# Performance work log

Measured on AMD Instinct MI355X. Metric: run time of the kernel, lower is better.

## Reference

```python
import jax, jax.numpy as jnp
import numpy as np

B, S, R, C_Q, C_KV, H, C_A = 1, 128, 256, 256, 256, 8, 32


def setup_inputs() -> dict:
    key = jax.random.key(0)
    ks = jax.random.split(key, 11)
    scale = 0.02
    q = jax.random.normal(ks[0], (B, S, R, C_Q), jnp.float32)
    kv = jax.random.normal(ks[1], (B, S, R, C_KV), jnp.float32)
    bias = jax.random.normal(ks[2], (B, 1, R, R, H), jnp.float32)
    bias_mask = jax.random.randint(ks[3], (B, S, R), 0, 2).astype(jnp.float32)
    w_q = jax.random.normal(ks[4], (C_Q, H, C_A), jnp.float32) * scale
    w_k = jax.random.normal(ks[5], (C_KV, H, C_A), jnp.float32) * scale
    w_v = jax.random.normal(ks[6], (C_KV, H, C_A), jnp.float32) * scale
    w_g = jax.random.normal(ks[7], (C_Q, H, C_A), jnp.float32) * scale
    b_g = jax.random.normal(ks[8], (H, C_A), jnp.float32) * scale
    w_o = jax.random.normal(ks[9], (H, C_A, C_Q), jnp.float32) * scale
    b_o = jax.random.normal(ks[10], (C_Q,), jnp.float32) * scale
    return {"q": q, "kv": kv, "bias": bias, "bias_mask": bias_mask,
            "w_q": w_q, "w_k": w_k, "w_v": w_v, "w_g": w_g, "b_g": b_g,
            "w_o": w_o, "b_o": b_o}


def reference(q, kv, bias, bias_mask, w_q, w_k, w_v, w_g, b_g, w_o, b_o):
    # q, kv: [B, S, R, C]; attention over residue dim R within each row s.
    c_a = w_q.shape[-1]
    normsize = 1.0 / jnp.sqrt(jnp.asarray(c_a, q.dtype))
    Q = jnp.einsum('bsqc,chd->bsqhd', q, w_q) * normsize  # [B,S,R,H,Ca]
    K = jnp.einsum('bskc,chd->bskhd', kv, w_k)
    V = jnp.einsum('bskc,chd->bskhd', kv, w_v)
    # affinity: [B,S,Q,K,H]
    AT = jnp.einsum('bsqhd,bskhd->bsqkh', Q, K)
    mask_bias = (bias_mask[:, :, None, :, None] - 1.0) * 1e9  # [B,S,1,K,1]
    AT = AT + bias + mask_bias
    AT = jax.nn.softmax(AT, axis=-2)  # softmax over K
    O = jnp.einsum('bsqkh,bskhd->bsqhd', AT, V)
    G = jax.nn.sigmoid(jnp.einsum('bsqc,chd->bsqhd', q, w_g) + b_g)
    O = O * G
    out = jnp.einsum('bsqhd,hdc->bsqc', O, w_o) + b_o  # [B,S,R,C_Q]
    return out
```

## Files before the change

### kernel.cpp

```cpp
#include <hip/hip_runtime.h>

typedef __bf16 bf16;
typedef __bf16 bf16x8 __attribute__((ext_vector_type(8)));
typedef __bf16 bf16x4 __attribute__((ext_vector_type(4)));
typedef float  f32x4  __attribute__((ext_vector_type(4)));
typedef unsigned int u32;
typedef unsigned int u32x2 __attribute__((ext_vector_type(2)));
typedef unsigned int u32x4 __attribute__((ext_vector_type(4)));
typedef unsigned short u16;

#define MFMA16(a, b, c) __builtin_amdgcn_mfma_f32_16x16x32_bf16((a), (b), (c), 0, 0, 0)
#define L2E 1.4426950408889634f


typedef __attribute__((address_space(3))) u32 lds_u32;
typedef const __attribute__((address_space(1))) u32 glob_u32;
__device__ __forceinline__ void gll16(const void* g, void* l) {
    __builtin_amdgcn_global_load_lds((glob_u32*)g, (lds_u32*)l, 16, 0, 0);
}

__device__ __forceinline__ u32 pk2(float lo, float hi) {
    u16 a = __builtin_bit_cast(u16, (bf16)lo);
    u16 b = __builtin_bit_cast(u16, (bf16)hi);
    return ((u32)b << 16) | (u32)a;
}

__device__ __forceinline__ bf16x8 cvt8(float4 a, float4 b) {
    bf16x8 t;
    t[0]=(bf16)a.x; t[1]=(bf16)a.y; t[2]=(bf16)a.z; t[3]=(bf16)a.w;
    t[4]=(bf16)b.x; t[5]=(bf16)b.y; t[6]=(bf16)b.z; t[7]=(bf16)b.w;
    return t;
}

__device__ __forceinline__ float fexp2(float x) {
#if __has_builtin(__builtin_amdgcn_exp2f)
    return __builtin_amdgcn_exp2f(x);
#else
    return exp2f(x);
#endif
}
__device__ __forceinline__ float frcp(float x) {
#if __has_builtin(__builtin_amdgcn_rcpf)
    return __builtin_amdgcn_rcpf(x);
#else
    return 1.0f / x;
#endif
}

__global__ __launch_bounds__(256) void prep_kernel(
    const float* __restrict__ bias,
    const float* __restrict__ w_q, const float* __restrict__ w_k,
    const float* __restrict__ w_v, const float* __restrict__ w_g,
    const float* __restrict__ w_o, const float* __restrict__ b_g,
    float* __restrict__ biasT,
    bf16* __restrict__ Wqg, bf16* __restrict__ Wkv, bf16* __restrict__ Wo,
    float* __restrict__ b_gL)
{
    const float norm = 0.17677669529663687f * L2E;
    const int gid = blockIdx.x * 256 + threadIdx.x;
    const int gsz = gridDim.x * 256;

    for (int u = gid; u < 524288; u += gsz) {
        int h = u >> 16, qq = (u >> 8) & 255, kk = u & 255;
        biasT[u] = bias[(((qq << 8) + kk) << 3) + h] * L2E;
    }
    for (int u = gid; u < 131072; u += gsz) {
        int n = u >> 8, k = u & 255;
        float v = (n < 256) ? w_q[k * 256 + n] * norm : w_g[k * 256 + (n - 256)] * L2E;
        Wqg[u] = (bf16)v;
    }
    for (int u = gid; u < 131072; u += gsz) {
        int n = u >> 8, k = u & 255;
        float v = (n < 256) ? w_k[k * 256 + n] : w_v[k * 256 + (n - 256)];
        Wkv[u] = (bf16)v;
    }
    for (int u = gid; u < 65536; u += gsz) {
        int n = u >> 8, k = u & 255;
        Wo[u] = (bf16)w_o[k * 256 + n];
    }
    for (int u = gid; u < 256; u += gsz) b_gL[u] = b_g[u] * L2E;
}

__device__ __forceinline__ void proj_core(
    const float* __restrict__ A32, const bf16* __restrict__ Bw,
    bf16* __restrict__ Cb, int m0, int n0)
{
    __shared__ __align__(16) bf16 As0[128 * 32], Bs0[128 * 32];
    __shared__ __align__(16) bf16 As1[128 * 32], Bs1[128 * 32];

    const int tid  = threadIdx.x;
    const int lane = tid & 63, wave = tid >> 6;
    const int quad = lane >> 4, lc = lane & 15;
    const int wr = wave >> 1, wc = wave & 1;

    const int r0 = tid >> 2, p0 = tid & 3;
    const size_t offA0 = (size_t)(m0 + r0) * 256 + p0 * 8;
    const size_t offA1 = (size_t)(m0 + 64 + r0) * 256 + p0 * 8;
    const bf16* gB0 = Bw + (size_t)(n0 + r0) * 256 + p0 * 8;
    const bf16* gB1 = Bw + (size_t)(n0 + 64 + r0) * 256 + p0 * 8;

    f32x4 acc[4][4];
    #pragma unroll
    for (int i = 0; i < 4; ++i)
        #pragma unroll
        for (int j = 0; j < 4; ++j) acc[i][j] = f32x4{0.f, 0.f, 0.f, 0.f};

    {
        float4 x0 = *(const float4*)(A32 + offA0);
        float4 x1 = *(const float4*)(A32 + offA0 + 4);
        float4 y0 = *(const float4*)(A32 + offA1);
        float4 y1 = *(const float4*)(A32 + offA1 + 4);
        *(bf16x8*)(As0 + tid * 8)         = cvt8(x0, x1);
        *(bf16x8*)(As0 + (tid + 256) * 8) = cvt8(y0, y1);
        gll16(gB0, Bs0 + tid * 8);
        gll16(gB1, Bs0 + (tid + 256) * 8);
    }
    __syncthreads();

    auto step = [&](const bf16* Ac, const bf16* Bc, bf16* An, bf16* Bn,
                    int kn, bool pf) {
        float4 x0, x1, y0, y1;
        if (pf) {
            x0 = *(const float4*)(A32 + offA0 + kn);
            x1 = *(const float4*)(A32 + offA0 + kn + 4);
            y0 = *(const float4*)(A32 + offA1 + kn);
            y1 = *(const float4*)(A32 + offA1 + kn + 4);
            gll16(gB0 + kn, Bn + tid * 8);
            gll16(gB1 + kn, Bn + (tid + 256) * 8);
        }
        __builtin_amdgcn_sched_barrier(0);

        bf16x8 aF[4], bF[4];
        #pragma unroll
        for (int mt = 0; mt < 4; ++mt)
            aF[mt] = *(const bf16x8*)(Ac + (wr * 64 + mt * 16 + lc) * 32 + quad * 8);
        #pragma unroll
        for (int nt = 0; nt < 4; ++nt)
            bF[nt] = *(const bf16x8*)(Bc + (wc * 64 + nt * 16 + lc) * 32 + quad * 8);
        #pragma unroll
        for (int mt = 0; mt < 4; ++mt)
            #pragma unroll
            for (int nt = 0; nt < 4; ++nt)
                acc[mt][nt] = MFMA16(aF[mt], bF[nt], acc[mt][nt]);

        if (pf) {
            *(bf16x8*)(An + tid * 8)         = cvt8(x0, x1);
            *(bf16x8*)(An + (tid + 256) * 8) = cvt8(y0, y1);
        }
        __syncthreads();
    };

    step(As0, Bs0, As1, Bs1,  32, true);
    step(As1, Bs1, As0, Bs0,  64, true);
    step(As0, Bs0, As1, Bs1,  96, true);
    step(As1, Bs1, As0, Bs0, 128, true);
    step(As0, Bs0, As1, Bs1, 160, true);
    step(As1, Bs1, As0, Bs0, 192, true);
    step(As0, Bs0, As1, Bs1, 224, true);
    step(As1, Bs1, As0, Bs0,   0, false);

    #pragma unroll
    for (int mt = 0; mt < 4; ++mt) {
        #pragma unroll
        for (int nt = 0; nt < 4; ++nt) {
            const int row = m0 + wr * 64 + mt * 16 + quad * 4;
            const int col = n0 + wc * 64 + nt * 16 + lc;
            #pragma unroll
            for (int rr = 0; rr < 4; ++rr)
                Cb[(size_t)(row + rr) * 512 + col] = (bf16)acc[mt][nt][rr];
        }
    }
}

__global__ __launch_bounds__(256) void proj_kernel(
    const float* __restrict__ qf, const float* __restrict__ kvf,
    const bf16* __restrict__ Wqg, const bf16* __restrict__ Wkv,
    bf16* __restrict__ QG, bf16* __restrict__ KV)
{
    int bid = blockIdx.x;
    bool sel = bid >= 1024;
    int b = bid & 1023;
    int strip = ((b >> 3) & 1) | ((b & 7) << 1) | (((b >> 4) & 15) << 4);
    int m0 = strip * 128, n0 = (b >> 8) * 128;
    proj_core(sel ? kvf : qf, sel ? Wkv : Wqg, sel ? KV : QG, m0, n0);
}

__global__ __launch_bounds__(256) void outproj_kernel(
    const bf16* __restrict__ OG, const bf16* __restrict__ Wo,
    const float* __restrict__ bo, float* __restrict__ out)
{
    __shared__ __align__(16) bf16 As0[64 * 32], Bs0[128 * 32];
    __shared__ __align__(16) bf16 As1[64 * 32], Bs1[128 * 32];

    const int bid = blockIdx.x;
    const int x = bid & 7;
    const int strip = ((bid >> 3) & 3) | (x << 2) | (((bid >> 5) & 15) << 5);
    const int m0 = strip * 64, n0 = (bid >> 9) * 128;

    const int tid  = threadIdx.x;
    const int lane = tid & 63, wave = tid >> 6;
    const int quad = lane >> 4, lc = lane & 15;
    const int wr = wave >> 1, wc = wave & 1;

    const int r0 = tid >> 2, p0 = tid & 3;
    const bf16* gA  = OG + (size_t)(m0 + r0) * 256 + p0 * 8;
    const bf16* gB0 = Wo + (size_t)(n0 + r0) * 256 + p0 * 8;
    const bf16* gB1 = Wo + (size_t)(n0 + 64 + r0) * 256 + p0 * 8;

    f32x4 acc[2][4];
    #pragma unroll
    for (int i = 0; i < 2; ++i)
        #pragma unroll
        for (int j = 0; j < 4; ++j) acc[i][j] = f32x4{0.f, 0.f, 0.f, 0.f};

    gll16(gA,  As0 + tid * 8);
    gll16(gB0, Bs0 + tid * 8);
    gll16(gB1, Bs0 + (tid + 256) * 8);
    __syncthreads();

    auto step = [&](const bf16* Ac, const bf16* Bc, bf16* An, bf16* Bn,
                    int kn, bool pf) {
        if (pf) {
            gll16(gA + kn,  An + tid * 8);
            gll16(gB0 + kn, Bn + tid * 8);
            gll16(gB1 + kn, Bn + (tid + 256) * 8);
        }
        __builtin_amdgcn_sched_barrier(0);

        bf16x8 aF[2], bF[4];
        #pragma unroll
        for (int mt = 0; mt < 2; ++mt)
            aF[mt] = *(const bf16x8*)(Ac + (wr * 32 + mt * 16 + lc) * 32 + quad * 8);
        #pragma unroll
        for (int nt = 0; nt < 4; ++nt)
            bF[nt] = *(const bf16x8*)(Bc + (wc * 64 + nt * 16 + lc) * 32 + quad * 8);
        #pragma unroll
        for (int mt = 0; mt < 2; ++mt)
            #pragma unroll
            for (int nt = 0; nt < 4; ++nt)
                acc[mt][nt] = MFMA16(aF[mt], bF[nt], acc[mt][nt]);
        __syncthreads();
    };

    step(As0, Bs0, As1, Bs1,  32, true);
    step(As1, Bs1, As0, Bs0,  64, true);
    step(As0, Bs0, As1, Bs1,  96, true);
    step(As1, Bs1, As0, Bs0, 128, true);
    step(As0, Bs0, As1, Bs1, 160, true);
    step(As1, Bs1, As0, Bs0, 192, true);
    step(As0, Bs0, As1, Bs1, 224, true);
    step(As1, Bs1, As0, Bs0,   0, false);

    #pragma unroll
    for (int mt = 0; mt < 2; ++mt) {
        #pragma unroll
        for (int nt = 0; nt < 4; ++nt) {
            const int row = m0 + wr * 32 + mt * 16 + quad * 4;
            const int col = n0 + wc * 64 + nt * 16 + lc;
            const float bb = bo[col];
            #pragma unroll
            for (int rr = 0; rr < 4; ++rr)
                out[(size_t)(row + rr) * 256 + col] = acc[mt][nt][rr] + bb;
        }
    }
}

#define A_OFF_MASK 0
#define A_OFF_K    1024
#define A_OFF_VT   21504
#define A_LDS_TOT  (21504 + 32 * 264 * 2)

__global__ __launch_bounds__(256) void attn_kernel(
    const bf16* __restrict__ QG, const bf16* __restrict__ KV,
    const float* __restrict__ biasT, const float* __restrict__ bias_mask,
    const float* __restrict__ b_gL, bf16* __restrict__ OG)
{
    __shared__ __align__(16) char smem[A_LDS_TOT];
    float* maskadd = (float*)(smem + A_OFF_MASK);
    bf16*  Ks      = (bf16*)(smem + A_OFF_K);
    bf16*  Vt      = (bf16*)(smem + A_OFF_VT);

    const int tid  = threadIdx.x;
    const int wave = tid >> 6, lane = tid & 63;
    const int quad = lane >> 4, lc = lane & 15;
    const int h = blockIdx.x >> 7;
    const int s = blockIdx.x & 127;

    maskadd[tid] = (bias_mask[s * 256 + tid] - 1.0f) * (1e9f * L2E);
    {
        const bf16* kvrow = KV + (size_t)(s * 256 + tid) * 512 + h * 32;
        #pragma unroll
        for (int j = 0; j < 4; ++j)
            *(bf16x8*)(Ks + tid * 40 + j * 8) = *(const bf16x8*)(kvrow + j * 8);
        bf16x8 vx[4];
        #pragma unroll
        for (int j = 0; j < 4; ++j) vx[j] = *(const bf16x8*)(kvrow + 256 + j * 8);
        #pragma unroll
        for (int d = 0; d < 32; ++d)
            Vt[d * 264 + tid] = vx[d >> 3][d & 7];
    }
    __syncthreads();

    const f32x4 bg0 = *(const f32x4*)(b_gL + h * 32 + quad * 4);
    const f32x4 bg1 = *(const f32x4*)(b_gL + h * 32 + 16 + quad * 4);

    #pragma unroll 1
    for (int p = 0; p < 4; ++p) {
        const int q0 = (wave * 4 + p) * 16;

        bf16x8 qf = *(const bf16x8*)(QG + (size_t)(s * 256 + q0 + lc) * 512 + h * 32 + quad * 8);

        const float* bT = biasT + (((size_t)h * 256 + q0 + lc) << 8) + quad * 4;
        u32x2 cw[16];
        float sum = 0.f;
        #pragma unroll
        for (int half = 0; half < 2; ++half) {
            f32x4 sc[8];
            #pragma unroll
            for (int k8 = 0; k8 < 8; ++k8) {
                const int kt = half * 8 + k8;
                bf16x8 kf = *(const bf16x8*)(Ks + (kt * 16 + lc) * 40 + quad * 8);
                f32x4 z = {0.f, 0.f, 0.f, 0.f};
                sc[k8] = MFMA16(kf, qf, z);
            }
            #pragma unroll
            for (int k8 = 0; k8 < 8; ++k8) {
                const int kt = half * 8 + k8;
                f32x4 bv = *(const f32x4*)(bT + kt * 16);
                f32x4 mv = *(const f32x4*)(maskadd + kt * 16 + quad * 4);
                f32x4 t = sc[k8] + bv + mv;
                float e0 = fexp2(t[0]);
                float e1 = fexp2(t[1]);
                float e2 = fexp2(t[2]);
                float e3 = fexp2(t[3]);
                sum += (e0 + e1) + (e2 + e3);
                cw[kt] = u32x2{pk2(e0, e1), pk2(e2, e3)};
            }
            __builtin_amdgcn_sched_barrier(0x6);
        }

        const bf16* gp = QG + (size_t)(s * 256 + q0 + lc) * 512 + 256 + h * 32 + quad * 4;
        bf16x4 gv0 = *(const bf16x4*)(gp);
        bf16x4 gv1 = *(const bf16x4*)(gp + 16);

        f32x4 o0 = {0.f, 0.f, 0.f, 0.f}, o1 = {0.f, 0.f, 0.f, 0.f};
        #pragma unroll
        for (int ks = 0; ks < 8; ++ks) {
            u32 c0 = cw[2 * ks].x,     c1 = cw[2 * ks].y;
            u32 c2 = cw[2 * ks + 1].x, c3 = cw[2 * ks + 1].y;
            u32x2 s02 = __builtin_amdgcn_permlane32_swap(c0, c2, false, false);
            u32x2 s13 = __builtin_amdgcn_permlane32_swap(c1, c3, false, false);
            u32x2 e02 = __builtin_amdgcn_permlane16_swap(s02.x, s02.y, false, false);
            u32x2 e13 = __builtin_amdgcn_permlane16_swap(s13.x, s13.y, false, false);
            u32x4 pw = {e02.x, e13.x, e02.y, e13.y};
            bf16x8 pf = __builtin_bit_cast(bf16x8, pw);
            bf16x8 v0 = *(const bf16x8*)(Vt + lc * 264 + ks * 32 + quad * 8);
            bf16x8 v1 = *(const bf16x8*)(Vt + (16 + lc) * 264 + ks * 32 + quad * 8);
            o0 = MFMA16(v0, pf, o0);
            o1 = MFMA16(v1, pf, o1);
        }

        sum += __shfl_xor(sum, 16, 64);
        sum += __shfl_xor(sum, 32, 64);
        const float inv = frcp(sum);

        bf16* op = OG + (size_t)(s * 256 + q0 + lc) * 256 + h * 32 + quad * 4;
        #pragma unroll
        for (int nt = 0; nt < 2; ++nt) {
            f32x4 ov = nt ? o1 : o0;
            f32x4 bg = nt ? bg1 : bg0;
            bf16x4 gv = nt ? gv1 : gv0;
            bf16x4 ob;
            #pragma unroll
            for (int rr = 0; rr < 4; ++rr) {
                float e = fexp2(-((float)gv[rr] + bg[rr]));
                float g = frcp(1.0f + e);
                ob[rr] = (bf16)(ov[rr] * (inv * g));
            }
            *(bf16x4*)(op + nt * 16) = ob;
        }
    }
}

extern "C" void kernel_launch(void* const* d_in, const int* in_sizes, int n_in,
                              void* d_out, int out_size, void* d_ws, size_t ws_size,
                              hipStream_t stream)
{
    (void)in_sizes; (void)n_in; (void)out_size; (void)ws_size;
    const float* q    = (const float*)d_in[0];
    const float* kv   = (const float*)d_in[1];
    const float* bias = (const float*)d_in[2];
    const float* mask = (const float*)d_in[3];
    const float* w_q  = (const float*)d_in[4];
    const float* w_k  = (const float*)d_in[5];
    const float* w_v  = (const float*)d_in[6];
    const float* w_g  = (const float*)d_in[7];
    const float* b_g  = (const float*)d_in[8];
    const float* w_o  = (const float*)d_in[9];
    const float* b_o  = (const float*)d_in[10];
    float* out = (float*)d_out;

    char* ws = (char*)d_ws;
    bf16*  OG    = (bf16*)(ws + 0);
    bf16*  QG    = (bf16*)(ws + 33554432);
    bf16*  KV    = (bf16*)(ws + 67108864);
    float* biasT = (float*)(ws + 100663296);
    bf16*  Wqg   = (bf16*)(ws + 102760448);
    bf16*  Wkv   = (bf16*)(ws + 103022592);
    bf16*  Wo    = (bf16*)(ws + 103284736);
    float* b_gL  = (float*)(ws + 103415808);

    prep_kernel<<<256, 256, 0, stream>>>(bias, w_q, w_k, w_v, w_g, w_o, b_g,
                                         biasT, Wqg, Wkv, Wo, b_gL);
    proj_kernel<<<2048, 256, 0, stream>>>(q, kv, Wqg, Wkv, QG, KV);
    attn_kernel<<<1024, 256, 0, stream>>>(QG, KV, biasT, mask, b_gL, OG);
    outproj_kernel<<<1024, 256, 0, stream>>>(OG, Wo, b_o, out);
}
```

Measured before the change: 208.6 us.

## Move bias/Wo prep into proj kernel, pad A LDS, head-major QG/KV layout

Only the Wqg/Wkv weight conversion stays in prep_kernel, which now runs on fewer blocks. The bias transpose, Wo conversion and b_g scaling move into 320 extra blocks of proj_kernel so they overlap with the projection GEMMs. The A-tile LDS rows are padded from 32 to 40 elements to reduce bank conflicts on fragment reads. The projection outputs are written head-major (per-head contiguous Q, G and KV slices), so the attention kernel reads compact 32- or 64-element rows instead of strided 512-wide rows. The trade-off is more scattered output stores in the projection epilogue and a larger, mixed-role grid for proj_kernel.

```diff
diff --git a/kernel.cpp b/kernel.cpp
--- a/kernel.cpp
+++ b/kernel.cpp
@@ -48,22 +48,14 @@
 }
 
 __global__ __launch_bounds__(256) void prep_kernel(
-    const float* __restrict__ bias,
     const float* __restrict__ w_q, const float* __restrict__ w_k,
     const float* __restrict__ w_v, const float* __restrict__ w_g,
-    const float* __restrict__ w_o, const float* __restrict__ b_g,
-    float* __restrict__ biasT,
-    bf16* __restrict__ Wqg, bf16* __restrict__ Wkv, bf16* __restrict__ Wo,
-    float* __restrict__ b_gL)
+    bf16* __restrict__ Wqg, bf16* __restrict__ Wkv)
 {
     const float norm = 0.17677669529663687f * L2E;
     const int gid = blockIdx.x * 256 + threadIdx.x;
     const int gsz = gridDim.x * 256;
 
-    for (int u = gid; u < 524288; u += gsz) {
-        int h = u >> 16, qq = (u >> 8) & 255, kk = u & 255;
-        biasT[u] = bias[(((qq << 8) + kk) << 3) + h] * L2E;
-    }
     for (int u = gid; u < 131072; u += gsz) {
         int n = u >> 8, k = u & 255;
         float v = (n < 256) ? w_q[k * 256 + n] * norm : w_g[k * 256 + (n - 256)] * L2E;
@@ -74,19 +66,14 @@
         float v = (n < 256) ? w_k[k * 256 + n] : w_v[k * 256 + (n - 256)];
         Wkv[u] = (bf16)v;
     }
-    for (int u = gid; u < 65536; u += gsz) {
-        int n = u >> 8, k = u & 255;
-        Wo[u] = (bf16)w_o[k * 256 + n];
-    }
-    for (int u = gid; u < 256; u += gsz) b_gL[u] = b_g[u] * L2E;
 }
 
 __device__ __forceinline__ void proj_core(
     const float* __restrict__ A32, const bf16* __restrict__ Bw,
-    bf16* __restrict__ Cb, int m0, int n0)
-{
-    __shared__ __align__(16) bf16 As0[128 * 32], Bs0[128 * 32];
-    __shared__ __align__(16) bf16 As1[128 * 32], Bs1[128 * 32];
+    bf16* __restrict__ Cb, int m0, int n0, bool kvmode)
+{
+    __shared__ __align__(16) bf16 As0[128 * 40], Bs0[128 * 32];
+    __shared__ __align__(16) bf16 As1[128 * 40], Bs1[128 * 32];
 
     const int tid  = threadIdx.x;
     const int lane = tid & 63, wave = tid >> 6;
@@ -98,6 +85,8 @@
     const size_t offA1 = (size_t)(m0 + 64 + r0) * 256 + p0 * 8;
     const bf16* gB0 = Bw + (size_t)(n0 + r0) * 256 + p0 * 8;
     const bf16* gB1 = Bw + (size_t)(n0 + 64 + r0) * 256 + p0 * 8;
+    const int aw0 = r0 * 40 + p0 * 8;
+    const int aw1 = (r0 + 64) * 40 + p0 * 8;
 
     f32x4 acc[4][4];
     #pragma unroll
@@ -110,8 +99,8 @@
         float4 x1 = *(const float4*)(A32 + offA0 + 4);
         float4 y0 = *(const float4*)(A32 + offA1);
         float4 y1 = *(const float4*)(A32 + offA1 + 4);
-        *(bf16x8*)(As0 + tid * 8)         = cvt8(x0, x1);
-        *(bf16x8*)(As0 + (tid + 256) * 8) = cvt8(y0, y1);
+        *(bf16x8*)(As0 + aw0) = cvt8(x0, x1);
+        *(bf16x8*)(As0 + aw1) = cvt8(y0, y1);
         gll16(gB0, Bs0 + tid * 8);
         gll16(gB1, Bs0 + (tid + 256) * 8);
     }
@@ -133,7 +122,7 @@
         bf16x8 aF[4], bF[4];
         #pragma unroll
         for (int mt = 0; mt < 4; ++mt)
-            aF[mt] = *(const bf16x8*)(Ac + (wr * 64 + mt * 16 + lc) * 32 + quad * 8);
+            aF[mt] = *(const bf16x8*)(Ac + (wr * 64 + mt * 16 + lc) * 40 + quad * 8);
         #pragma unroll
         for (int nt = 0; nt < 4; ++nt)
             bF[nt] = *(const bf16x8*)(Bc + (wc * 64 + nt * 16 + lc) * 32 + quad * 8);
@@ -144,8 +133,8 @@
                 acc[mt][nt] = MFMA16(aF[mt], bF[nt], acc[mt][nt]);
 
         if (pf) {
-            *(bf16x8*)(An + tid * 8)         = cvt8(x0, x1);
-            *(bf16x8*)(An + (tid + 256) * 8) = cvt8(y0, y1);
+            *(bf16x8*)(An + aw0) = cvt8(x0, x1);
+            *(bf16x8*)(An + aw1) = cvt8(y0, y1);
         }
         __syncthreads();
     };
@@ -164,10 +153,21 @@
         #pragma unroll
         for (int nt = 0; nt < 4; ++nt) {
             const int row = m0 + wr * 64 + mt * 16 + quad * 4;
-            const int col = n0 + wc * 64 + nt * 16 + lc;
-            #pragma unroll
-            for (int rr = 0; rr < 4; ++rr)
-                Cb[(size_t)(row + rr) * 512 + col] = (bf16)acc[mt][nt][rr];
+            const int colbase = n0 + wc * 64 + nt * 16;
+            const int slice = colbase >> 5;
+            const int cin = (colbase & 16) + lc;
+            if (!kvmode) {
+                bf16* dst = Cb + ((size_t)slice << 20) + ((size_t)row << 5) + cin;
+                #pragma unroll
+                for (int rr = 0; rr < 4; ++rr)
+                    dst[rr * 32] = (bf16)acc[mt][nt][rr];
+            } else {
+                const int hh = slice & 7, vofs = (slice >> 3) * 32;
+                bf16* dst = Cb + ((size_t)hh << 21) + ((size_t)row << 6) + vofs + cin;
+                #pragma unroll
+                for (int rr = 0; rr < 4; ++rr)
+                    dst[rr * 64] = (bf16)acc[mt][nt][rr];
+            }
         }
     }
 }
@@ -175,14 +175,31 @@
 __global__ __launch_bounds__(256) void proj_kernel(
     const float* __restrict__ qf, const float* __restrict__ kvf,
     const bf16* __restrict__ Wqg, const bf16* __restrict__ Wkv,
-    bf16* __restrict__ QG, bf16* __restrict__ KV)
+    bf16* __restrict__ QG, bf16* __restrict__ KV,
+    const float* __restrict__ bias, const float* __restrict__ w_o,
+    const float* __restrict__ b_g,
+    float* __restrict__ biasT, bf16* __restrict__ Wo, float* __restrict__ b_gL)
 {
     int bid = blockIdx.x;
+    if (bid >= 2048) {
+        const int gid = (bid - 2048) * 256 + threadIdx.x;
+        const int gsz = 320 * 256;
+        for (int u = gid; u < 524288; u += gsz) {
+            int h = u >> 16, qq = (u >> 8) & 255, kk = u & 255;
+            biasT[u] = bias[(((qq << 8) + kk) << 3) + h] * L2E;
+        }
+        for (int u = gid; u < 65536; u += gsz) {
+            int n = u >> 8, k = u & 255;
+            Wo[u] = (bf16)w_o[k * 256 + n];
+        }
+        if (gid < 256) b_gL[gid] = b_g[gid] * L2E;
+        return;
+    }
     bool sel = bid >= 1024;
     int b = bid & 1023;
     int strip = ((b >> 3) & 1) | ((b & 7) << 1) | (((b >> 4) & 15) << 4);
     int m0 = strip * 128, n0 = (b >> 8) * 128;
-    proj_core(sel ? kvf : qf, sel ? Wkv : Wqg, sel ? KV : QG, m0, n0);
+    proj_core(sel ? kvf : qf, sel ? Wkv : Wqg, sel ? KV : QG, m0, n0, sel);
 }
 
 __global__ __launch_bounds__(256) void outproj_kernel(
@@ -286,15 +303,19 @@
     const int h = blockIdx.x >> 7;
     const int s = blockIdx.x & 127;
 
+    const bf16* Qh  = QG + ((size_t)h << 20);
+    const bf16* Gh  = QG + ((size_t)(8 + h) << 20);
+    const bf16* KVh = KV + ((size_t)h << 21);
+
     maskadd[tid] = (bias_mask[s * 256 + tid] - 1.0f) * (1e9f * L2E);
     {
-        const bf16* kvrow = KV + (size_t)(s * 256 + tid) * 512 + h * 32;
+        const bf16* kvrow = KVh + (size_t)(s * 256 + tid) * 64;
         #pragma unroll
         for (int j = 0; j < 4; ++j)
             *(bf16x8*)(Ks + tid * 40 + j * 8) = *(const bf16x8*)(kvrow + j * 8);
         bf16x8 vx[4];
         #pragma unroll
-        for (int j = 0; j < 4; ++j) vx[j] = *(const bf16x8*)(kvrow + 256 + j * 8);
+        for (int j = 0; j < 4; ++j) vx[j] = *(const bf16x8*)(kvrow + 32 + j * 8);
         #pragma unroll
         for (int d = 0; d < 32; ++d)
             Vt[d * 264 + tid] = vx[d >> 3][d & 7];
@@ -308,7 +329,7 @@
     for (int p = 0; p < 4; ++p) {
         const int q0 = (wave * 4 + p) * 16;
 
-        bf16x8 qf = *(const bf16x8*)(QG + (size_t)(s * 256 + q0 + lc) * 512 + h * 32 + quad * 8);
+        bf16x8 qf = *(const bf16x8*)(Qh + (size_t)(s * 256 + q0 + lc) * 32 + quad * 8);
 
         const float* bT = biasT + (((size_t)h * 256 + q0 + lc) << 8) + quad * 4;
         u32x2 cw[16];
@@ -339,7 +360,7 @@
             __builtin_amdgcn_sched_barrier(0x6);
         }
 
-        const bf16* gp = QG + (size_t)(s * 256 + q0 + lc) * 512 + 256 + h * 32 + quad * 4;
+        const bf16* gp = Gh + (size_t)(s * 256 + q0 + lc) * 32 + quad * 4;
         bf16x4 gv0 = *(const bf16x4*)(gp);
         bf16x4 gv1 = *(const bf16x4*)(gp + 16);
 
@@ -410,9 +431,9 @@
     bf16*  Wo    = (bf16*)(ws + 103284736);
     float* b_gL  = (float*)(ws + 103415808);
 
-    prep_kernel<<<256, 256, 0, stream>>>(bias, w_q, w_k, w_v, w_g, w_o, b_g,
-                                         biasT, Wqg, Wkv, Wo, b_gL);
-    proj_kernel<<<2048, 256, 0, stream>>>(q, kv, Wqg, Wkv, QG, KV);
+    prep_kernel<<<64, 256, 0, stream>>>(w_q, w_k, w_v, w_g, Wqg, Wkv);
+    proj_kernel<<<2368, 256, 0, stream>>>(q, kv, Wqg, Wkv, QG, KV,
+                                          bias, w_o, b_g, biasT, Wo, b_gL);
     attn_kernel<<<1024, 256, 0, stream>>>(QG, KV, biasT, mask, b_gL, OG);
     outproj_kernel<<<1024, 256, 0, stream>>>(OG, Wo, b_o, out);
 }
```

Measured after the change: 217.8 us. 1.04x slower.

## Move bias transpose and Wo prep into extra projection blocks

Applied to the files above, without the earlier changes.

The bias transpose, Wo conversion and b_g scaling move out of the serial prep kernel into 64 extra blocks appended to the projection launch, so they overlap with the projection GEMM. The bias transpose is also rewritten to read eight contiguous floats per element with vector loads and scatter them to the eight head planes. The prep kernel shrinks to 64 blocks handling only the Wqg and Wkv weights. The extra blocks are scheduled last and compete with the GEMM blocks for bandwidth, and their scattered writes are less coalesced per plane.

```diff
diff --git a/kernel.cpp b/kernel.cpp
--- a/kernel.cpp
+++ b/kernel.cpp
@@ -48,22 +48,14 @@
 }
 
 __global__ __launch_bounds__(256) void prep_kernel(
-    const float* __restrict__ bias,
     const float* __restrict__ w_q, const float* __restrict__ w_k,
     const float* __restrict__ w_v, const float* __restrict__ w_g,
-    const float* __restrict__ w_o, const float* __restrict__ b_g,
-    float* __restrict__ biasT,
-    bf16* __restrict__ Wqg, bf16* __restrict__ Wkv, bf16* __restrict__ Wo,
-    float* __restrict__ b_gL)
+    bf16* __restrict__ Wqg, bf16* __restrict__ Wkv)
 {
     const float norm = 0.17677669529663687f * L2E;
     const int gid = blockIdx.x * 256 + threadIdx.x;
     const int gsz = gridDim.x * 256;
 
-    for (int u = gid; u < 524288; u += gsz) {
-        int h = u >> 16, qq = (u >> 8) & 255, kk = u & 255;
-        biasT[u] = bias[(((qq << 8) + kk) << 3) + h] * L2E;
-    }
     for (int u = gid; u < 131072; u += gsz) {
         int n = u >> 8, k = u & 255;
         float v = (n < 256) ? w_q[k * 256 + n] * norm : w_g[k * 256 + (n - 256)] * L2E;
@@ -74,11 +66,6 @@
         float v = (n < 256) ? w_k[k * 256 + n] : w_v[k * 256 + (n - 256)];
         Wkv[u] = (bf16)v;
     }
-    for (int u = gid; u < 65536; u += gsz) {
-        int n = u >> 8, k = u & 255;
-        Wo[u] = (bf16)w_o[k * 256 + n];
-    }
-    for (int u = gid; u < 256; u += gsz) b_gL[u] = b_g[u] * L2E;
 }
 
 __device__ __forceinline__ void proj_core(
@@ -175,9 +162,34 @@
 __global__ __launch_bounds__(256) void proj_kernel(
     const float* __restrict__ qf, const float* __restrict__ kvf,
     const bf16* __restrict__ Wqg, const bf16* __restrict__ Wkv,
-    bf16* __restrict__ QG, bf16* __restrict__ KV)
+    bf16* __restrict__ QG, bf16* __restrict__ KV,
+    const float* __restrict__ bias, const float* __restrict__ w_o,
+    const float* __restrict__ b_g,
+    float* __restrict__ biasT, bf16* __restrict__ Wo, float* __restrict__ b_gL)
 {
     int bid = blockIdx.x;
+    if (bid >= 2048) {
+        const int gid = (bid - 2048) * 256 + threadIdx.x;
+        const int gsz = 64 * 256;
+        for (int u = gid; u < 65536; u += gsz) {
+            float4 a = *(const float4*)(bias + (size_t)u * 8);
+            float4 b = *(const float4*)(bias + (size_t)u * 8 + 4);
+            biasT[          u] = a.x * L2E;
+            biasT[ 65536 + u] = a.y * L2E;
+            biasT[131072 + u] = a.z * L2E;
+            biasT[196608 + u] = a.w * L2E;
+            biasT[262144 + u] = b.x * L2E;
+            biasT[327680 + u] = b.y * L2E;
+            biasT[393216 + u] = b.z * L2E;
+            biasT[458752 + u] = b.w * L2E;
+        }
+        for (int u = gid; u < 65536; u += gsz) {
+            int n = u >> 8, k = u & 255;
+            Wo[u] = (bf16)w_o[k * 256 + n];
+        }
+        if (gid < 256) b_gL[gid] = b_g[gid] * L2E;
+        return;
+    }
     bool sel = bid >= 1024;
     int b = bid & 1023;
     int strip = ((b >> 3) & 1) | ((b & 7) << 1) | (((b >> 4) & 15) << 4);
@@ -410,9 +422,9 @@
     bf16*  Wo    = (bf16*)(ws + 103284736);
     float* b_gL  = (float*)(ws + 103415808);
 
-    prep_kernel<<<256, 256, 0, stream>>>(bias, w_q, w_k, w_v, w_g, w_o, b_g,
-                                         biasT, Wqg, Wkv, Wo, b_gL);
-    proj_kernel<<<2048, 256, 0, stream>>>(q, kv, Wqg, Wkv, QG, KV);
+    prep_kernel<<<64, 256, 0, stream>>>(w_q, w_k, w_v, w_g, Wqg, Wkv);
+    proj_kernel<<<2112, 256, 0, stream>>>(q, kv, Wqg, Wkv, QG, KV,
+                                          bias, w_o, b_g, biasT, Wo, b_gL);
     attn_kernel<<<1024, 256, 0, stream>>>(QG, KV, biasT, mask, b_gL, OG);
     outproj_kernel<<<1024, 256, 0, stream>>>(OG, Wo, b_o, out);
 }
```

Measured after the change: 213.5 us. 1.02x slower.
